# Kernel optimization log

Measured on AMD Instinct MI355X. Metric: run time of the kernel, lower is better.

The kernel has to match this reference:

```python
import jax, jax.numpy as jnp
import numpy as np

NUM_EXPERTS = 8
HIDDEN = 1024
INTERMEDIATE = 2816
TOTAL_TOKENS = 4096  # 512 tokens per expert


def setup_inputs() -> dict:
    key = jax.random.key(0)
    k_x, k1, k2, k3 = jax.random.split(key, 4)
    hiddens = jax.random.normal(k_x, (TOTAL_TOKENS, HIDDEN), dtype=jnp.float32)
    # tokens assumed pre-sorted by expert; equal-sized groups here
    batch_sizes = jnp.full((NUM_EXPERTS,), TOTAL_TOKENS // NUM_EXPERTS, dtype=jnp.int64)
    w1_weight = jax.random.normal(k1, (NUM_EXPERTS, HIDDEN, INTERMEDIATE), dtype=jnp.float32)
    w2_weight = jax.random.normal(k2, (NUM_EXPERTS, INTERMEDIATE, HIDDEN), dtype=jnp.float32)
    w3_weight = jax.random.normal(k3, (NUM_EXPERTS, HIDDEN, INTERMEDIATE), dtype=jnp.float32)
    return {
        "hiddens": hiddens,
        "w1_weight": w1_weight,
        "w2_weight": w2_weight,
        "w3_weight": w3_weight,
        "batch_sizes": batch_sizes,
    }


def _grouped_moe(hiddens, w1, w2, w3, batch_sizes):
    """Grouped SwiGLU FFN: tokens are contiguous per expert (sizes = batch_sizes).

    Jit-safe formulation: map each token to its expert id, then run one masked
    dense GEMM trio per expert (small fixed expert count). Zero rows contribute
    exactly zero (silu(0)*0 == 0), so no final masking of the output is needed.
    """
    num_experts = w1.shape[0]
    total_tokens = hiddens.shape[0]
    bounds = jnp.cumsum(batch_sizes)  # [E] exclusive-right boundaries
    expert_ids = jnp.searchsorted(bounds, jnp.arange(total_tokens), side="right")  # [T]
    out = jnp.zeros((total_tokens, w2.shape[-1]), dtype=hiddens.dtype)
    for e in range(num_experts):
        mask = (expert_ids == e)[:, None]  # [T, 1]
        xe = jnp.where(mask, hiddens, 0)   # zero out other experts' tokens
        up = jax.nn.silu(xe @ w1[e]) * (xe @ w3[e])  # [T, F] SwiGLU
        out = out + up @ w2[e]             # [T, H]
    return out


def reference(hiddens, w1_weight, w2_weight, w3_weight, batch_sizes):
    return _grouped_moe(hiddens, w1_weight, w2_weight, w3_weight, batch_sizes)
```

## Files before the change

kernel.cpp:

```cpp
#include <hip/hip_runtime.h>
#include <hip/hip_bf16.h>

#define NE 8
#define HD 1024
#define ID 2816
#define TT 4096
#define BM 128
#define BK 32
#define BN1 64
#define BN2 64
#define NTH 256
#define MAXMT (TT / BM + NE)

typedef __attribute__((ext_vector_type(4))) float f32x4;
typedef __attribute__((ext_vector_type(8))) short s16x8;
typedef __attribute__((ext_vector_type(4))) short s16x4;

__device__ __forceinline__ unsigned int f2bfpk(float lo, float hi) {
  float2 t; t.x = lo; t.y = hi;
  union { __hip_bfloat162 h2; unsigned int u; } cv;
  cv.h2 = __float22bfloat162_rn(t);
  return cv.u;
}

__device__ __forceinline__ void lds_barrier() {
  asm volatile("s_waitcnt lgkmcnt(0)" ::: "memory");
  __builtin_amdgcn_s_barrier();
}

__device__ __forceinline__ bool map_tile(const void* bsp, int mt, int& e,
                                         int& mstart, int& rowend) {
  const int* w = (const int*)bsp;
  bool is64 = (w[1] == 0) && (w[3] == 0) && (w[5] == 0) && (w[7] == 0) &&
              ((w[0] | w[2] | w[4] | w[6]) != 0);
  long long start = 0;
  int rem = mt;
  for (int i = 0; i < NE; ++i) {
    long long b = is64 ? ((const long long*)bsp)[i] : (long long)w[i];
    if (b < 0) b = 0;
    int tiles = (int)((b + BM - 1) / BM);
    if (rem < tiles) {
      long long m0 = start + (long long)rem * BM;
      long long me = start + b;
      if (m0 >= TT) return false;
      if (me > TT) me = TT;
      e = i; mstart = (int)m0; rowend = (int)me;
      return true;
    }
    rem -= tiles;
    start += b;
  }
  return false;
}

__global__ __launch_bounds__(NTH) void cvt_x(const float* __restrict__ x,
                                             __hip_bfloat16* __restrict__ xb) {
  size_t i = ((size_t)blockIdx.x * NTH + threadIdx.x) * 8;
  f32x4 v0 = *(const f32x4*)(x + i);
  f32x4 v1 = *(const f32x4*)(x + i + 4);
  s16x8 o;
  unsigned int p0 = f2bfpk(v0[0], v0[1]), p1 = f2bfpk(v0[2], v0[3]);
  unsigned int p2 = f2bfpk(v1[0], v1[1]), p3 = f2bfpk(v1[2], v1[3]);
  o[0] = (short)(p0 & 0xffff); o[1] = (short)(p0 >> 16);
  o[2] = (short)(p1 & 0xffff); o[3] = (short)(p1 >> 16);
  o[4] = (short)(p2 & 0xffff); o[5] = (short)(p2 >> 16);
  o[6] = (short)(p3 & 0xffff); o[7] = (short)(p3 >> 16);
  *(s16x8*)((unsigned short*)xb + i) = o;
}

__global__ __launch_bounds__(NTH, 2) void moe_gemm1(
    const __hip_bfloat16* __restrict__ xbf, const float* __restrict__ w1,
    const float* __restrict__ w3, const void* __restrict__ bsp,
    __hip_bfloat16* __restrict__ up) {
  __shared__ __align__(16) char As[2][BM * 80];
  __shared__ __align__(16) char B1s[2][BN1 * 72];
  __shared__ __align__(16) char B3s[2][BN1 * 72];

  const int NWG = (ID / BN1) * MAXMT;
  int bid = blockIdx.x;
  int logical = (bid & 7) * (NWG >> 3) + (bid >> 3);
  int mt = logical % MAXMT;
  int nt = logical / MAXMT;
  int e, mstart, rowend;
  if (!map_tile(bsp, mt, e, mstart, rowend)) return;
  const int n0 = nt * BN1;
  const int tid = threadIdx.x;

  const int lane = tid & 63;
  const int wv = tid >> 6;
  const int wr = wv >> 1, wc = wv & 1;
  const int q = lane >> 4, r16 = lane & 15;

  const int a_k8 = (tid & 3) * 8;
  const int a_r0 = tid >> 2;
  const int b_n = tid & 63;
  const int b_kp0 = tid >> 6;

  const bool ok0 = (mstart + a_r0) < rowend;
  const bool ok1 = (mstart + a_r0 + 64) < rowend;

  const __hip_bfloat16* xc = xbf + (size_t)(mstart + a_r0) * HD + a_k8;
  const float* w1c = w1 + (size_t)e * HD * ID + n0 + b_n + (size_t)(2 * b_kp0) * ID;
  const float* w3c = w3 + (size_t)e * HD * ID + n0 + b_n + (size_t)(2 * b_kp0) * ID;

  f32x4 acc1[4][2], acc3[4][2];
#pragma unroll
  for (int i = 0; i < 4; ++i)
#pragma unroll
    for (int j = 0; j < 2; ++j) { acc1[i][j] = (f32x4)0.f; acc3[i][j] = (f32x4)0.f; }

  s16x8 A0[2], A1[2];
  float W1a[4][2], W3a[4][2], W1b[4][2], W3b[4][2];

  auto load_t = [&](s16x8* A, float (*W1_)[2], float (*W3_)[2]) {
    A[0] = ok0 ? *(const s16x8*)xc : (s16x8)0;
    A[1] = ok1 ? *(const s16x8*)(xc + (size_t)64 * HD) : (s16x8)0;
    xc += BK;
#pragma unroll
    for (int i = 0; i < 4; ++i) {
      const float* p1 = w1c + (size_t)(8 * i) * ID;
      W1_[i][0] = p1[0]; W1_[i][1] = p1[ID];
      const float* p3 = w3c + (size_t)(8 * i) * ID;
      W3_[i][0] = p3[0]; W3_[i][1] = p3[ID];
    }
    w1c += (size_t)BK * ID; w3c += (size_t)BK * ID;
  };
  auto store_t = [&](char* As_, char* B1_, char* B3_, const s16x8* A,
                     const float (*W1_)[2], const float (*W3_)[2]) {
    *(s16x8*)(As_ + a_r0 * 80 + a_k8 * 2) = A[0];
    *(s16x8*)(As_ + (a_r0 + 64) * 80 + a_k8 * 2) = A[1];
#pragma unroll
    for (int i = 0; i < 4; ++i) {
      int kp = b_kp0 + i * 4;
      *(unsigned int*)(B1_ + b_n * 72 + kp * 4) = f2bfpk(W1_[i][0], W1_[i][1]);
      *(unsigned int*)(B3_ + b_n * 72 + kp * 4) = f2bfpk(W3_[i][0], W3_[i][1]);
    }
  };
  auto compute_t = [&](const char* As_, const char* B1_, const char* B3_) {
    s16x8 a[4], b1[2], b3[2];
#pragma unroll
    for (int i = 0; i < 4; ++i)
      a[i] = *(const s16x8*)(As_ + (wr * 64 + i * 16 + r16) * 80 + q * 16);
#pragma unroll
    for (int j = 0; j < 2; ++j) {
      const char* p1 = B1_ + (wc * 32 + j * 16 + r16) * 72 + q * 16;
      s16x4 l1 = *(const s16x4*)p1, h1 = *(const s16x4*)(p1 + 8);
      b1[j] = __builtin_shufflevector(l1, h1, 0, 1, 2, 3, 4, 5, 6, 7);
      const char* p3 = B3_ + (wc * 32 + j * 16 + r16) * 72 + q * 16;
      s16x4 l3 = *(const s16x4*)p3, h3 = *(const s16x4*)(p3 + 8);
      b3[j] = __builtin_shufflevector(l3, h3, 0, 1, 2, 3, 4, 5, 6, 7);
    }
#pragma unroll
    for (int i = 0; i < 4; ++i)
#pragma unroll
      for (int j = 0; j < 2; ++j) {
        acc1[i][j] = __builtin_amdgcn_mfma_f32_16x16x32_bf16(a[i], b1[j], acc1[i][j], 0, 0, 0);
        acc3[i][j] = __builtin_amdgcn_mfma_f32_16x16x32_bf16(a[i], b3[j], acc3[i][j], 0, 0, 0);
      }
  };

  const int NK = HD / BK;
  load_t(A0, W1a, W3a);
  load_t(A1, W1b, W3b);
  store_t(As[0], B1s[0], B3s[0], A0, W1a, W3a);
  lds_barrier();
  for (int kt = 0; kt < NK; kt += 2) {
    if (kt + 2 < NK) load_t(A0, W1a, W3a);
    compute_t(As[0], B1s[0], B3s[0]);
    store_t(As[1], B1s[1], B3s[1], A1, W1b, W3b);
    lds_barrier();
    if (kt + 3 < NK) load_t(A1, W1b, W3b);
    compute_t(As[1], B1s[1], B3s[1]);
    if (kt + 2 < NK) {
      store_t(As[0], B1s[0], B3s[0], A0, W1a, W3a);
      lds_barrier();
    }
  }

#pragma unroll
  for (int i = 0; i < 4; ++i)
#pragma unroll
    for (int r = 0; r < 4; ++r) {
      int gm = mstart + wr * 64 + i * 16 + q * 4 + r;
      if (gm < rowend) {
#pragma unroll
        for (int j = 0; j < 2; ++j) {
          float v1 = acc1[i][j][r], v3 = acc3[i][j][r];
          float s = v1 / (1.f + __expf(-v1));
          up[(size_t)gm * ID + n0 + wc * 32 + j * 16 + r16] = __float2bfloat16(s * v3);
        }
      }
    }
}

__global__ __launch_bounds__(NTH, 2) void moe_gemm2(
    const __hip_bfloat16* __restrict__ up, const float* __restrict__ w2,
    const void* __restrict__ bsp, float* __restrict__ out) {
  __shared__ __align__(16) char As[2][BM * 80];
  __shared__ __align__(16) char Bs[2][BN2 * 72];

  const int NWG = (HD / BN2) * MAXMT;
  int bid = blockIdx.x;
  int logical = (bid & 7) * (NWG >> 3) + (bid >> 3);
  int mt = logical % MAXMT;
  int nt = logical / MAXMT;
  int e, mstart, rowend;
  if (!map_tile(bsp, mt, e, mstart, rowend)) return;
  const int n0 = nt * BN2;
  const int tid = threadIdx.x;

  const int lane = tid & 63;
  const int wv = tid >> 6;
  const int wr = wv >> 1, wc = wv & 1;
  const int q = lane >> 4, r16 = lane & 15;

  const int a_k8 = (tid & 3) * 8;
  const int a_r0 = tid >> 2;
  const int b_n = tid & 63;
  const int b_kp0 = tid >> 6;

  const bool ok0 = (mstart + a_r0) < rowend;
  const bool ok1 = (mstart + a_r0 + 64) < rowend;

  const __hip_bfloat16* uc = up + (size_t)(mstart + a_r0) * ID + a_k8;
  const float* w2c = w2 + (size_t)e * ID * HD + n0 + b_n + (size_t)(2 * b_kp0) * HD;

  f32x4 acc[4][2];
#pragma unroll
  for (int i = 0; i < 4; ++i)
#pragma unroll
    for (int j = 0; j < 2; ++j) acc[i][j] = (f32x4)0.f;

  s16x8 A0[2], A1[2];
  float Wa[4][2], Wb[4][2];

  auto load_t = [&](s16x8* A, float (*W_)[2]) {
    A[0] = ok0 ? *(const s16x8*)uc : (s16x8)0;
    A[1] = ok1 ? *(const s16x8*)(uc + (size_t)64 * ID) : (s16x8)0;
    uc += BK;
#pragma unroll
    for (int i = 0; i < 4; ++i) {
      const float* p = w2c + (size_t)(8 * i) * HD;
      W_[i][0] = p[0]; W_[i][1] = p[HD];
    }
    w2c += (size_t)BK * HD;
  };
  auto store_t = [&](char* As_, char* B_, const s16x8* A, const float (*W_)[2]) {
    *(s16x8*)(As_ + a_r0 * 80 + a_k8 * 2) = A[0];
    *(s16x8*)(As_ + (a_r0 + 64) * 80 + a_k8 * 2) = A[1];
#pragma unroll
    for (int i = 0; i < 4; ++i) {
      int kp = b_kp0 + i * 4;
      *(unsigned int*)(B_ + b_n * 72 + kp * 4) = f2bfpk(W_[i][0], W_[i][1]);
    }
  };
  auto compute_t = [&](const char* As_, const char* B_) {
    s16x8 a[4], b[2];
#pragma unroll
    for (int i = 0; i < 4; ++i)
      a[i] = *(const s16x8*)(As_ + (wr * 64 + i * 16 + r16) * 80 + q * 16);
#pragma unroll
    for (int j = 0; j < 2; ++j) {
      const char* p = B_ + (wc * 32 + j * 16 + r16) * 72 + q * 16;
      s16x4 lo = *(const s16x4*)p, hi = *(const s16x4*)(p + 8);
      b[j] = __builtin_shufflevector(lo, hi, 0, 1, 2, 3, 4, 5, 6, 7);
    }
#pragma unroll
    for (int i = 0; i < 4; ++i)
#pragma unroll
      for (int j = 0; j < 2; ++j)
        acc[i][j] = __builtin_amdgcn_mfma_f32_16x16x32_bf16(a[i], b[j], acc[i][j], 0, 0, 0);
  };

  const int NK = ID / BK;
  load_t(A0, Wa);
  load_t(A1, Wb);
  store_t(As[0], Bs[0], A0, Wa);
  lds_barrier();
  for (int kt = 0; kt < NK; kt += 2) {
    if (kt + 2 < NK) load_t(A0, Wa);
    compute_t(As[0], Bs[0]);
    store_t(As[1], Bs[1], A1, Wb);
    lds_barrier();
    if (kt + 3 < NK) load_t(A1, Wb);
    compute_t(As[1], Bs[1]);
    if (kt + 2 < NK) {
      store_t(As[0], Bs[0], A0, Wa);
      lds_barrier();
    }
  }

#pragma unroll
  for (int i = 0; i < 4; ++i)
#pragma unroll
    for (int r = 0; r < 4; ++r) {
      int gm = mstart + wr * 64 + i * 16 + q * 4 + r;
      if (gm < rowend) {
#pragma unroll
        for (int j = 0; j < 2; ++j)
          out[(size_t)gm * HD + n0 + wc * 32 + j * 16 + r16] = acc[i][j][r];
      }
    }
}

extern "C" void kernel_launch(void* const* d_in, const int* in_sizes, int n_in,
                              void* d_out, int out_size, void* d_ws, size_t ws_size,
                              hipStream_t stream) {
  const float* x = (const float*)d_in[0];
  const float* w1 = (const float*)d_in[1];
  const float* w2 = (const float*)d_in[2];
  const float* w3 = (const float*)d_in[3];
  const void* bs = d_in[4];
  float* out = (float*)d_out;
  __hip_bfloat16* xbf = (__hip_bfloat16*)d_ws;
  __hip_bfloat16* up = (__hip_bfloat16*)((char*)d_ws + (size_t)TT * HD * 2);

  hipMemsetAsync(d_out, 0, (size_t)out_size * sizeof(float), stream);

  dim3 blk(NTH);
  cvt_x<<<dim3(TT * HD / (8 * NTH)), blk, 0, stream>>>(x, xbf);
  moe_gemm1<<<dim3((ID / BN1) * MAXMT), blk, 0, stream>>>(xbf, w1, w3, bs, up);
  moe_gemm2<<<dim3((HD / BN2) * MAXMT), blk, 0, stream>>>(up, w2, bs, out);
}
```

Measured before the change: 195.3 us.

## Widen GEMM1 N-tile to 128 with 512 threads and vectorize B-tile LDS access

GEMM1 now uses 128-column tiles and 8 waves (512 threads) per workgroup, so each staged A tile of activations is reused across twice as many output columns. Both GEMMs restage the converted weight tiles with an 80-byte row pitch. Each thread converts four consecutive-k weights and writes them with one 64-bit LDS store, and the MFMA B operands are read with a single 128-bit load instead of two 64-bit loads plus a shuffle. Launch bounds are raised to request higher occupancy, which may cap registers per thread and cause spills, and the wider tiles mean fewer workgroups in GEMM1.

```diff
diff --git a/kernel.cpp b/kernel.cpp
--- a/kernel.cpp
+++ b/kernel.cpp
@@ -7,14 +7,12 @@
 #define TT 4096
 #define BM 128
 #define BK 32
-#define BN1 64
+#define BN1 128
 #define BN2 64
-#define NTH 256
 #define MAXMT (TT / BM + NE)
 
 typedef __attribute__((ext_vector_type(4))) float f32x4;
 typedef __attribute__((ext_vector_type(8))) short s16x8;
-typedef __attribute__((ext_vector_type(4))) short s16x4;
 
 __device__ __forceinline__ unsigned int f2bfpk(float lo, float hi) {
   float2 t; t.x = lo; t.y = hi;
@@ -53,9 +51,9 @@
   return false;
 }
 
-__global__ __launch_bounds__(NTH) void cvt_x(const float* __restrict__ x,
+__global__ __launch_bounds__(256) void cvt_x(const float* __restrict__ x,
                                              __hip_bfloat16* __restrict__ xb) {
-  size_t i = ((size_t)blockIdx.x * NTH + threadIdx.x) * 8;
+  size_t i = ((size_t)blockIdx.x * 256 + threadIdx.x) * 8;
   f32x4 v0 = *(const f32x4*)(x + i);
   f32x4 v1 = *(const f32x4*)(x + i + 4);
   s16x8 o;
@@ -68,13 +66,13 @@
   *(s16x8*)((unsigned short*)xb + i) = o;
 }
 
-__global__ __launch_bounds__(NTH, 2) void moe_gemm1(
+__global__ __launch_bounds__(512, 4) void moe_gemm1(
     const __hip_bfloat16* __restrict__ xbf, const float* __restrict__ w1,
     const float* __restrict__ w3, const void* __restrict__ bsp,
     __hip_bfloat16* __restrict__ up) {
   __shared__ __align__(16) char As[2][BM * 80];
-  __shared__ __align__(16) char B1s[2][BN1 * 72];
-  __shared__ __align__(16) char B3s[2][BN1 * 72];
+  __shared__ __align__(16) char B1s[2][BN1 * 80];
+  __shared__ __align__(16) char B3s[2][BN1 * 80];
 
   const int NWG = (ID / BN1) * MAXMT;
   int bid = blockIdx.x;
@@ -88,20 +86,19 @@
 
   const int lane = tid & 63;
   const int wv = tid >> 6;
-  const int wr = wv >> 1, wc = wv & 1;
+  const int wr = wv >> 2, wc = wv & 3;
   const int q = lane >> 4, r16 = lane & 15;
 
   const int a_k8 = (tid & 3) * 8;
   const int a_r0 = tid >> 2;
-  const int b_n = tid & 63;
-  const int b_kp0 = tid >> 6;
+  const int b_n = tid & 127;
+  const int b_kq = tid >> 7;
 
   const bool ok0 = (mstart + a_r0) < rowend;
-  const bool ok1 = (mstart + a_r0 + 64) < rowend;
 
   const __hip_bfloat16* xc = xbf + (size_t)(mstart + a_r0) * HD + a_k8;
-  const float* w1c = w1 + (size_t)e * HD * ID + n0 + b_n + (size_t)(2 * b_kp0) * ID;
-  const float* w3c = w3 + (size_t)e * HD * ID + n0 + b_n + (size_t)(2 * b_kp0) * ID;
+  const float* w1c = w1 + (size_t)e * HD * ID + (size_t)(4 * b_kq) * ID + n0 + b_n;
+  const float* w3c = w3 + (size_t)e * HD * ID + (size_t)(4 * b_kq) * ID + n0 + b_n;
 
   f32x4 acc1[4][2], acc3[4][2];
 #pragma unroll
@@ -109,31 +106,34 @@
 #pragma unroll
     for (int j = 0; j < 2; ++j) { acc1[i][j] = (f32x4)0.f; acc3[i][j] = (f32x4)0.f; }
 
-  s16x8 A0[2], A1[2];
-  float W1a[4][2], W3a[4][2], W1b[4][2], W3b[4][2];
-
-  auto load_t = [&](s16x8* A, float (*W1_)[2], float (*W3_)[2]) {
-    A[0] = ok0 ? *(const s16x8*)xc : (s16x8)0;
-    A[1] = ok1 ? *(const s16x8*)(xc + (size_t)64 * HD) : (s16x8)0;
+  s16x8 A0, A1;
+  float W1a[2][4], W3a[2][4], W1b[2][4], W3b[2][4];
+
+  auto load_t = [&](s16x8& A, float (*W1_)[4], float (*W3_)[4]) {
+    A = ok0 ? *(const s16x8*)xc : (s16x8)0;
     xc += BK;
 #pragma unroll
-    for (int i = 0; i < 4; ++i) {
-      const float* p1 = w1c + (size_t)(8 * i) * ID;
-      W1_[i][0] = p1[0]; W1_[i][1] = p1[ID];
-      const float* p3 = w3c + (size_t)(8 * i) * ID;
-      W3_[i][0] = p3[0]; W3_[i][1] = p3[ID];
-    }
+    for (int g = 0; g < 2; ++g)
+#pragma unroll
+      for (int kk = 0; kk < 4; ++kk) {
+        W1_[g][kk] = w1c[(size_t)(g * 16 + kk) * ID];
+        W3_[g][kk] = w3c[(size_t)(g * 16 + kk) * ID];
+      }
     w1c += (size_t)BK * ID; w3c += (size_t)BK * ID;
   };
-  auto store_t = [&](char* As_, char* B1_, char* B3_, const s16x8* A,
-                     const float (*W1_)[2], const float (*W3_)[2]) {
-    *(s16x8*)(As_ + a_r0 * 80 + a_k8 * 2) = A[0];
-    *(s16x8*)(As_ + (a_r0 + 64) * 80 + a_k8 * 2) = A[1];
-#pragma unroll
-    for (int i = 0; i < 4; ++i) {
-      int kp = b_kp0 + i * 4;
-      *(unsigned int*)(B1_ + b_n * 72 + kp * 4) = f2bfpk(W1_[i][0], W1_[i][1]);
-      *(unsigned int*)(B3_ + b_n * 72 + kp * 4) = f2bfpk(W3_[i][0], W3_[i][1]);
+  auto store_t = [&](char* As_, char* B1_, char* B3_, const s16x8& A,
+                     const float (*W1_)[4], const float (*W3_)[4]) {
+    *(s16x8*)(As_ + a_r0 * 80 + a_k8 * 2) = A;
+#pragma unroll
+    for (int g = 0; g < 2; ++g) {
+      unsigned long long p1 =
+          (unsigned long long)f2bfpk(W1_[g][0], W1_[g][1]) |
+          ((unsigned long long)f2bfpk(W1_[g][2], W1_[g][3]) << 32);
+      *(unsigned long long*)(B1_ + b_n * 80 + b_kq * 8 + g * 32) = p1;
+      unsigned long long p3 =
+          (unsigned long long)f2bfpk(W3_[g][0], W3_[g][1]) |
+          ((unsigned long long)f2bfpk(W3_[g][2], W3_[g][3]) << 32);
+      *(unsigned long long*)(B3_ + b_n * 80 + b_kq * 8 + g * 32) = p3;
     }
   };
   auto compute_t = [&](const char* As_, const char* B1_, const char* B3_) {
@@ -143,12 +143,8 @@
       a[i] = *(const s16x8*)(As_ + (wr * 64 + i * 16 + r16) * 80 + q * 16);
 #pragma unroll
     for (int j = 0; j < 2; ++j) {
-      const char* p1 = B1_ + (wc * 32 + j * 16 + r16) * 72 + q * 16;
-      s16x4 l1 = *(const s16x4*)p1, h1 = *(const s16x4*)(p1 + 8);
-      b1[j] = __builtin_shufflevector(l1, h1, 0, 1, 2, 3, 4, 5, 6, 7);
-      const char* p3 = B3_ + (wc * 32 + j * 16 + r16) * 72 + q * 16;
-      s16x4 l3 = *(const s16x4*)p3, h3 = *(const s16x4*)(p3 + 8);
-      b3[j] = __builtin_shufflevector(l3, h3, 0, 1, 2, 3, 4, 5, 6, 7);
+      b1[j] = *(const s16x8*)(B1_ + (wc * 32 + j * 16 + r16) * 80 + q * 16);
+      b3[j] = *(const s16x8*)(B3_ + (wc * 32 + j * 16 + r16) * 80 + q * 16);
     }
 #pragma unroll
     for (int i = 0; i < 4; ++i)
@@ -193,11 +189,11 @@
     }
 }
 
-__global__ __launch_bounds__(NTH, 2) void moe_gemm2(
+__global__ __launch_bounds__(256, 4) void moe_gemm2(
     const __hip_bfloat16* __restrict__ up, const float* __restrict__ w2,
     const void* __restrict__ bsp, float* __restrict__ out) {
   __shared__ __align__(16) char As[2][BM * 80];
-  __shared__ __align__(16) char Bs[2][BN2 * 72];
+  __shared__ __align__(16) char Bs[2][BN2 * 80];
 
   const int NWG = (HD / BN2) * MAXMT;
   int bid = blockIdx.x;
@@ -217,13 +213,13 @@
   const int a_k8 = (tid & 3) * 8;
   const int a_r0 = tid >> 2;
   const int b_n = tid & 63;
-  const int b_kp0 = tid >> 6;
+  const int b_kq = tid >> 6;
 
   const bool ok0 = (mstart + a_r0) < rowend;
   const bool ok1 = (mstart + a_r0 + 64) < rowend;
 
   const __hip_bfloat16* uc = up + (size_t)(mstart + a_r0) * ID + a_k8;
-  const float* w2c = w2 + (size_t)e * ID * HD + n0 + b_n + (size_t)(2 * b_kp0) * HD;
+  const float* w2c = w2 + (size_t)e * ID * HD + (size_t)(4 * b_kq) * HD + n0 + b_n;
 
   f32x4 acc[4][2];
 #pragma unroll
@@ -232,26 +228,28 @@
     for (int j = 0; j < 2; ++j) acc[i][j] = (f32x4)0.f;
 
   s16x8 A0[2], A1[2];
-  float Wa[4][2], Wb[4][2];
-
-  auto load_t = [&](s16x8* A, float (*W_)[2]) {
+  float Wa[2][4], Wb[2][4];
+
+  auto load_t = [&](s16x8* A, float (*W_)[4]) {
     A[0] = ok0 ? *(const s16x8*)uc : (s16x8)0;
     A[1] = ok1 ? *(const s16x8*)(uc + (size_t)64 * ID) : (s16x8)0;
     uc += BK;
 #pragma unroll
-    for (int i = 0; i < 4; ++i) {
-      const float* p = w2c + (size_t)(8 * i) * HD;
-      W_[i][0] = p[0]; W_[i][1] = p[HD];
-    }
+    for (int g = 0; g < 2; ++g)
+#pragma unroll
+      for (int kk = 0; kk < 4; ++kk)
+        W_[g][kk] = w2c[(size_t)(g * 16 + kk) * HD];
     w2c += (size_t)BK * HD;
   };
-  auto store_t = [&](char* As_, char* B_, const s16x8* A, const float (*W_)[2]) {
+  auto store_t = [&](char* As_, char* B_, const s16x8* A, const float (*W_)[4]) {
     *(s16x8*)(As_ + a_r0 * 80 + a_k8 * 2) = A[0];
     *(s16x8*)(As_ + (a_r0 + 64) * 80 + a_k8 * 2) = A[1];
 #pragma unroll
-    for (int i = 0; i < 4; ++i) {
-      int kp = b_kp0 + i * 4;
-      *(unsigned int*)(B_ + b_n * 72 + kp * 4) = f2bfpk(W_[i][0], W_[i][1]);
+    for (int g = 0; g < 2; ++g) {
+      unsigned long long p =
+          (unsigned long long)f2bfpk(W_[g][0], W_[g][1]) |
+          ((unsigned long long)f2bfpk(W_[g][2], W_[g][3]) << 32);
+      *(unsigned long long*)(B_ + b_n * 80 + b_kq * 8 + g * 32) = p;
     }
   };
   auto compute_t = [&](const char* As_, const char* B_) {
@@ -260,11 +258,8 @@
     for (int i = 0; i < 4; ++i)
       a[i] = *(const s16x8*)(As_ + (wr * 64 + i * 16 + r16) * 80 + q * 16);
 #pragma unroll
-    for (int j = 0; j < 2; ++j) {
-      const char* p = B_ + (wc * 32 + j * 16 + r16) * 72 + q * 16;
-      s16x4 lo = *(const s16x4*)p, hi = *(const s16x4*)(p + 8);
-      b[j] = __builtin_shufflevector(lo, hi, 0, 1, 2, 3, 4, 5, 6, 7);
-    }
+    for (int j = 0; j < 2; ++j)
+      b[j] = *(const s16x8*)(B_ + (wc * 32 + j * 16 + r16) * 80 + q * 16);
 #pragma unroll
     for (int i = 0; i < 4; ++i)
 #pragma unroll
@@ -317,8 +312,7 @@
 
   hipMemsetAsync(d_out, 0, (size_t)out_size * sizeof(float), stream);
 
-  dim3 blk(NTH);
-  cvt_x<<<dim3(TT * HD / (8 * NTH)), blk, 0, stream>>>(x, xbf);
-  moe_gemm1<<<dim3((ID / BN1) * MAXMT), blk, 0, stream>>>(xbf, w1, w3, bs, up);
-  moe_gemm2<<<dim3((HD / BN2) * MAXMT), blk, 0, stream>>>(up, w2, bs, out);
-}
+  cvt_x<<<dim3(TT * HD / (8 * 256)), dim3(256), 0, stream>>>(x, xbf);
+  moe_gemm1<<<dim3((ID / BN1) * MAXMT), dim3(512), 0, stream>>>(xbf, w1, w3, bs, up);
+  moe_gemm2<<<dim3((HD / BN2) * MAXMT), dim3(256), 0, stream>>>(up, w2, bs, out);
+}
```

Measured after the change: 469.9 us. 141% more time.
